# Kernel optimization log

Measured on AMD Instinct MI355X. Metric: run time of the kernel, lower is better.

## Reference

```python
import jax, jax.numpy as jnp
import numpy as np

B, T, C, H = 2, 2048, 768, 12
D = C // H              # head_dim = 64
LOCAL_WINDOW = 256
LN_EPS = 1e-5


def _layernorm(x, w, b):
    mu = jnp.mean(x, axis=-1, keepdims=True)
    var = jnp.var(x, axis=-1, keepdims=True)
    return (x - mu) * jax.lax.rsqrt(var + LN_EPS) * w + b


def setup_inputs() -> dict:
    key = jax.random.key(0)
    ks = jax.random.split(key, 8)
    inp = {
        "x": jax.random.normal(ks[0], (B, T, C), dtype=jnp.float32),
        "mamba_raw": jax.random.normal(ks[1], (B, T, C), dtype=jnp.float32),
        # c_attn / c_proj per nn.init in __init__
        "c_attn_w": 0.02 * jax.random.normal(ks[2], (C, 3 * C), dtype=jnp.float32),
        "c_attn_b": jnp.zeros((3 * C,), dtype=jnp.float32),
        "c_proj_w": 0.02 * jax.random.normal(ks[3], (C, C), dtype=jnp.float32),
        "c_proj_b": jnp.zeros((C,), dtype=jnp.float32),
        "ln_w": jnp.ones((C,), dtype=jnp.float32),
        "ln_b": jnp.zeros((C,), dtype=jnp.float32),
        "mamba_scale": jnp.asarray(0.1, dtype=jnp.float32),
        "sel_w": 0.01 * jax.random.normal(ks[4], (C, 1), dtype=jnp.float32),
        "sel_b": jnp.zeros((1,), dtype=jnp.float32),
        "local_weight": jnp.asarray(0.5, dtype=jnp.float32),
        "global_weight": jnp.asarray(0.5, dtype=jnp.float32),
    }
    return inp


def reference(x, mamba_raw, c_attn_w, c_attn_b, c_proj_w, c_proj_b,
              ln_w, ln_b, mamba_scale, sel_w, sel_b, local_weight, global_weight):
    scale = D ** -0.5
    qkv = x @ c_attn_w + c_attn_b                       # (B,T,3C)
    q, k, v = jnp.split(qkv, 3, axis=-1)
    q = q.reshape(B, T, H, D)
    k = k.reshape(B, T, H, D)
    v = v.reshape(B, T, H, D)

    scores = jnp.einsum('bihd,bjhd->bhij', q, k) * scale  # (B,H,T,T)
    i = jnp.arange(T)[:, None]
    j = jnp.arange(T)[None, :]
    causal = j > i                                       # mask strictly-future keys
    neg_inf = jnp.asarray(-jnp.inf, dtype=scores.dtype)
    scores = jnp.where(causal, neg_inf, scores)

    # frozen mamba branch (mamba_raw is a constant activation)
    mamba_raw = jax.lax.stop_gradient(mamba_raw)
    mamba_scaled = mamba_scale * _layernorm(mamba_raw, ln_w, ln_b)   # (B,T,C)
    sel = jax.nn.sigmoid(mamba_scaled @ sel_w + sel_b)               # (B,T,1)
    sel = sel[:, None, :, 0][:, :, None, :]                          # (B,1,1,T) over keys

    attn_global = scores * (0.5 + 0.5 * sel)             # -inf stays -inf

    outside_local = j < jnp.maximum(i - LOCAL_WINDOW, 0)
    attn_local = jnp.where(outside_local, neg_inf, scores)

    w_l = jax.nn.sigmoid(local_weight)
    w_g = jax.nn.sigmoid(global_weight)
    w_sum = w_l + w_g
    w_l, w_g = w_l / w_sum, w_g / w_sum

    attn_combined = w_l * jax.nn.softmax(attn_local, axis=-1) \
                  + w_g * jax.nn.softmax(attn_global, axis=-1)

    out = jnp.einsum('bhij,bjhd->bihd', attn_combined, v).reshape(B, T, C)
    return out @ c_proj_w + c_proj_b
```

## Files before the change

### kernel.cpp

```cpp
#include <hip/hip_runtime.h>
#include <math.h>

#define Bsz 2
#define Tsz 2048
#define Csz 768
#define Hsz 12
#define C3  2304
#define WIN 256
#define LN_EPS 1e-5f

#define QSCALE 0.1803368801111137f

typedef short bf16x8 __attribute__((ext_vector_type(8)));
typedef float f32x4  __attribute__((ext_vector_type(4)));

__device__ __forceinline__ unsigned short f2b(float f) {
    unsigned int u = __float_as_uint(f);
    u = (u + 0x7fffu + ((u >> 16) & 1u)) >> 16;
    return (unsigned short)u;
}

__device__ __forceinline__ float fast_exp2(float x) {
    float r;
    asm("v_exp_f32 %0, %1" : "=v"(r) : "v"(x));
    return r;
}

__global__ __launch_bounds__(256) void prep_fused(
    const float* __restrict__ x, unsigned short* __restrict__ xb,
    const float* __restrict__ c_attn_w, unsigned short* __restrict__ wq,
    const float* __restrict__ c_proj_w, unsigned short* __restrict__ wp,
    const float* __restrict__ mr, const float* __restrict__ ln_w,
    const float* __restrict__ ln_b, const float* __restrict__ scale_p,
    const float* __restrict__ sel_w, const float* __restrict__ sel_b,
    float* __restrict__ sel)
{
    __shared__ float tile[32][33];
    __shared__ float red1[256];
    __shared__ float red2[256];
    __shared__ float mu_sh, rstd_sh;

    const int blk = blockIdx.x;
    const int tid = threadIdx.x;

    if (blk < 3072) {
        int idx = blk * 256 + tid;
        float4 v = *(const float4*)(x + (size_t)idx * 4);
        unsigned int lo = (unsigned int)f2b(v.x) | ((unsigned int)f2b(v.y) << 16);
        unsigned int hi = (unsigned int)f2b(v.z) | ((unsigned int)f2b(v.w) << 16);
        uint2 o; o.x = lo; o.y = hi;
        *(uint2*)(xb + (size_t)idx * 4) = o;
        return;
    }
    if (blk < 5376) {
        const float* src; unsigned short* dst; int K, N, n0, k0;
        if (blk < 4800) {
            int i = blk - 3072;
            src = c_attn_w; dst = wq; K = Csz; N = C3;
            n0 = (i % 72) * 32; k0 = (i / 72) * 32;
        } else {
            int i = blk - 4800;
            src = c_proj_w; dst = wp; K = Csz; N = Csz;
            n0 = (i % 24) * 32; k0 = (i / 24) * 32;
        }
        const int tx = tid & 31, ty = tid >> 5;
        #pragma unroll
        for (int p = 0; p < 4; ++p)
            tile[ty + p * 8][tx] = src[(size_t)(k0 + ty + p * 8) * N + n0 + tx];
        __syncthreads();
        #pragma unroll
        for (int p = 0; p < 4; ++p)
            dst[(size_t)(n0 + ty + p * 8) * K + k0 + tx] = f2b(tile[tx][ty + p * 8]);
        return;
    }

    const int r = blk - 5376;
    const float* row = mr + (size_t)r * Csz;

    float s = 0.f, s2 = 0.f;
    for (int c = tid; c < Csz; c += 256) {
        float xv = row[c];
        s += xv; s2 += xv * xv;
    }
    red1[tid] = s; red2[tid] = s2;
    __syncthreads();
    for (int st = 128; st > 0; st >>= 1) {
        if (tid < st) { red1[tid] += red1[tid + st]; red2[tid] += red2[tid + st]; }
        __syncthreads();
    }
    if (tid == 0) {
        float mu = red1[0] * (1.f / Csz);
        float var = red2[0] * (1.f / Csz) - mu * mu;
        mu_sh = mu;
        rstd_sh = rsqrtf(var + LN_EPS);
    }
    __syncthreads();
    const float mu = mu_sh, rstd = rstd_sh;

    float dot = 0.f;
    for (int c = tid; c < Csz; c += 256) {
        float xn = (row[c] - mu) * rstd * ln_w[c] + ln_b[c];
        dot += xn * sel_w[c];
    }
    red1[tid] = dot;
    __syncthreads();
    for (int st = 128; st > 0; st >>= 1) {
        if (tid < st) red1[tid] += red1[tid + st];
        __syncthreads();
    }
    if (tid == 0) {
        float z = scale_p[0] * red1[0] + sel_b[0];
        sel[r] = 0.5f + 0.5f / (1.f + __expf(-z));
    }
}

template<int MODE>
__global__ __launch_bounds__(256) void gemm_bt_mfma(
    const unsigned short* __restrict__ A, const unsigned short* __restrict__ BT,
    const float* __restrict__ bias, void* __restrict__ Cout,
    unsigned short* __restrict__ KP, unsigned short* __restrict__ VP,
    int M, int N, int K)
{
    __shared__ unsigned short As[128 * 32];
    __shared__ unsigned short Bs[128 * 32];

    const int tid = threadIdx.x;
    const int lane = tid & 63, widx = tid >> 6;
    const int lm = lane & 15, quad = lane >> 4;
    const int wm = widx >> 1, wn = widx & 1;
    const int m0 = blockIdx.y * 128, n0 = blockIdx.x * 128;

    f32x4 acc[4][4];
    #pragma unroll
    for (int mt = 0; mt < 4; ++mt)
        #pragma unroll
        for (int nt = 0; nt < 4; ++nt)
            acc[mt][nt] = f32x4{0.f, 0.f, 0.f, 0.f};

    int rowS[2], cS[2];
    #pragma unroll
    for (int t = 0; t < 2; ++t) {
        int idx = t * 256 + tid;
        rowS[t] = idx >> 2;
        cS[t] = idx & 3;
    }

    bf16x8 pa[2], pb[2];
    #pragma unroll
    for (int t = 0; t < 2; ++t) {
        pa[t] = *(const bf16x8*)(A + (size_t)(m0 + rowS[t]) * K + cS[t] * 8);
        pb[t] = *(const bf16x8*)(BT + (size_t)(n0 + rowS[t]) * K + cS[t] * 8);
    }

    const int nk = K / 32;
    for (int kt = 0; kt < nk; ++kt) {
        __syncthreads();
        #pragma unroll
        for (int t = 0; t < 2; ++t) {
            *(bf16x8*)(&As[rowS[t] * 32 + ((cS[t] ^ ((rowS[t] >> 1) & 3)) << 3)]) = pa[t];
            *(bf16x8*)(&Bs[rowS[t] * 32 + ((cS[t] ^ ((rowS[t] >> 1) & 3)) << 3)]) = pb[t];
        }
        __syncthreads();
        if (kt + 1 < nk) {
            int k0 = (kt + 1) * 32;
            #pragma unroll
            for (int t = 0; t < 2; ++t) {
                pa[t] = *(const bf16x8*)(A + (size_t)(m0 + rowS[t]) * K + k0 + cS[t] * 8);
                pb[t] = *(const bf16x8*)(BT + (size_t)(n0 + rowS[t]) * K + k0 + cS[t] * 8);
            }
        }
        bf16x8 af[4], bf[4];
        #pragma unroll
        for (int mt = 0; mt < 4; ++mt) {
            int m = wm * 64 + mt * 16 + lm;
            af[mt] = *(const bf16x8*)(&As[m * 32 + ((quad ^ ((m >> 1) & 3)) << 3)]);
        }
        #pragma unroll
        for (int nt = 0; nt < 4; ++nt) {
            int n = wn * 64 + nt * 16 + lm;
            bf[nt] = *(const bf16x8*)(&Bs[n * 32 + ((quad ^ ((n >> 1) & 3)) << 3)]);
        }
        #pragma unroll
        for (int mt = 0; mt < 4; ++mt)
            #pragma unroll
            for (int nt = 0; nt < 4; ++nt)
                acc[mt][nt] = __builtin_amdgcn_mfma_f32_16x16x32_bf16(
                    af[mt], bf[nt], acc[mt][nt], 0, 0, 0);
    }

    float bv[4];
    #pragma unroll
    for (int nt = 0; nt < 4; ++nt)
        bv[nt] = bias[n0 + wn * 64 + nt * 16 + lm];

    #pragma unroll
    for (int mt = 0; mt < 4; ++mt) {
        #pragma unroll
        for (int nt = 0; nt < 4; ++nt) {
            const int cb = n0 + wn * 64 + nt * 16;
            const int col = cb + lm;
            const int rbase = m0 + wm * 64 + mt * 16 + quad * 4;
            if (MODE == 0) {
                #pragma unroll
                for (int r = 0; r < 4; ++r)
                    ((float*)Cout)[(size_t)(rbase + r) * N + col] =
                        acc[mt][nt][r] + bv[nt];
            } else if (cb < Csz) {
                #pragma unroll
                for (int r = 0; r < 4; ++r)
                    ((unsigned short*)Cout)[(size_t)(rbase + r) * Csz + col] =
                        f2b((acc[mt][nt][r] + bv[nt]) * QSCALE);
            } else if (cb < 2 * Csz) {
                const int dfull = col - Csz;
                const int h = dfull >> 6, dd = dfull & 63;
                const int f = dd >> 5, qd = (dd >> 3) & 3, j = dd & 7;
                #pragma unroll
                for (int r = 0; r < 4; ++r) {
                    const int row = rbase + r;
                    const int b = row >> 11, t = row & 2047;
                    const int ktk = t >> 4, lmk = t & 15;
                    size_t addr = ((((size_t)((b * Hsz + h) * 128 + ktk)) * 2 + f) * 512)
                                  + (qd * 16 + lmk) * 8 + j;
                    KP[addr] = f2b(acc[mt][nt][r] + bv[nt]);
                }
            } else {
                const int dfull = col - 2 * Csz;
                const int h = dfull >> 6, dd = dfull & 63;
                const int ntv = dd >> 4, lmv = dd & 15;
                #pragma unroll
                for (int r = 0; r < 4; ++r) {
                    const int row = rbase + r;
                    const int b = row >> 11, t = row & 2047;
                    const int jtv = t >> 5, qv = (t >> 3) & 3, j = t & 7;
                    size_t addr = (((size_t)((b * Hsz + h) * 64 + jtv) * 4 + ntv) * 512)
                                  + (qv * 16 + lmv) * 8 + j;
                    VP[addr] = f2b(acc[mt][nt][r] + bv[nt]);
                }
            }
        }
    }
}

__global__ __launch_bounds__(256) void attn_mfma(
    const unsigned short* __restrict__ qb, const unsigned short* __restrict__ KP,
    const unsigned short* __restrict__ VP, const float* __restrict__ fsel_arr,
    const float* __restrict__ lw_p, const float* __restrict__ gw_p,
    unsigned short* __restrict__ attnb)
{
    __shared__ __align__(16) unsigned char SMEM[18432];

    const int tid = threadIdx.x;
    const int widx = tid >> 6, lane = tid & 63;
    const int lm = lane & 15, quad = lane >> 4;

    unsigned short* Pg = (unsigned short*)SMEM + (widx * 2 + 0) * (16 * 72);
    unsigned short* Pl = (unsigned short*)SMEM + (widx * 2 + 1) * (16 * 72);
    float* MrgF = (float*)SMEM;
    #define MRG(slot, br, row, col) MrgF[((((slot) * 2 + (br)) * 16 + (row)) * 66) + (col)]

    const int strip = 127 - (int)(blockIdx.x / 24);
    const int bh = (int)(blockIdx.x % 24);
    const int h = bh % Hsz, b = bh / Hsz;
    const int i0 = strip * 16;

    const unsigned short* KPb = KP + (size_t)bh * 131072 + lane * 8;
    const unsigned short* VPb = VP + (size_t)bh * 131072 + lane * 8;

    const unsigned short* qrow =
        qb + (size_t)(b * Tsz + i0 + lm) * Csz + h * 64 + quad * 8;
    const bf16x8 qf0 = *(const bf16x8*)qrow;
    const bf16x8 qf1 = *(const bf16x8*)(qrow + 32);

    float l_g[4], l_l[4];
    f32x4 Og[4], Ol[4];
    #pragma unroll
    for (int r = 0; r < 4; ++r) { l_g[r] = 0.f; l_l[r] = 0.f; }
    #pragma unroll
    for (int nt = 0; nt < 4; ++nt) {
        Og[nt] = f32x4{0.f, 0.f, 0.f, 0.f};
        Ol[nt] = f32x4{0.f, 0.f, 0.f, 0.f};
    }

    const int jtd = i0 >> 6;
    const int jtl = (jtd - 4) > 0 ? (jtd - 4) : 0;

    for (int jt = widx; jt <= jtd; jt += 4) {
        const int j0 = jt * 64;
        const bool diag = (jt == jtd);
        const bool firstloc = (jt == jtl) && !diag;
        const bool loc = (jt >= jtl);

        const unsigned short* kp = KPb + (size_t)(j0 >> 4) * 1024;
        bf16x8 kc0[4], kc1[4];
        #pragma unroll
        for (int nt = 0; nt < 4; ++nt) {
            kc0[nt] = *(const bf16x8*)(kp + nt * 1024);
            kc1[nt] = *(const bf16x8*)(kp + nt * 1024 + 512);
        }

        f32x4 s[4];
        #pragma unroll
        for (int nt = 0; nt < 4; ++nt) {
            f32x4 z = f32x4{0.f, 0.f, 0.f, 0.f};
            z = __builtin_amdgcn_mfma_f32_16x16x32_bf16(qf0, kc0[nt], z, 0, 0, 0);
            z = __builtin_amdgcn_mfma_f32_16x16x32_bf16(qf1, kc1[nt], z, 0, 0, 0);
            s[nt] = z;
        }

        float fs[4];
        #pragma unroll
        for (int nt = 0; nt < 4; ++nt)
            fs[nt] = fsel_arr[b * Tsz + j0 + nt * 16 + lm];

        if (diag) {
            #pragma unroll
            for (int r = 0; r < 4; ++r) {
                const int qi = i0 + quad * 4 + r;
                #pragma unroll
                for (int nt = 0; nt < 4; ++nt) {
                    const int kj = j0 + nt * 16 + lm;
                    float p = fast_exp2(s[nt][r] * fs[nt]);
                    p = (kj > qi) ? 0.f : p;
                    unsigned int u = __float_as_uint(p);
                    l_g[r] += __uint_as_float(u & 0xffff0000u);
                    Pg[(quad * 4 + r) * 72 + nt * 16 + lm] = (unsigned short)(u >> 16);
                }
            }
        } else {
            #pragma unroll
            for (int r = 0; r < 4; ++r)
                #pragma unroll
                for (int nt = 0; nt < 4; ++nt) {
                    float p = fast_exp2(s[nt][r] * fs[nt]);
                    unsigned int u = __float_as_uint(p);
                    l_g[r] += __uint_as_float(u & 0xffff0000u);
                    Pg[(quad * 4 + r) * 72 + nt * 16 + lm] = (unsigned short)(u >> 16);
                }
        }

        if (loc) {
            if (diag) {
                #pragma unroll
                for (int r = 0; r < 4; ++r) {
                    const int qi = i0 + quad * 4 + r;
                    #pragma unroll
                    for (int nt = 0; nt < 4; ++nt) {
                        const int kj = j0 + nt * 16 + lm;
                        float p = fast_exp2(s[nt][r]);
                        p = (kj > qi || kj < qi - WIN) ? 0.f : p;
                        unsigned int u = __float_as_uint(p);
                        l_l[r] += __uint_as_float(u & 0xffff0000u);
                        Pl[(quad * 4 + r) * 72 + nt * 16 + lm] = (unsigned short)(u >> 16);
                    }
                }
            } else if (firstloc) {
                #pragma unroll
                for (int r = 0; r < 4; ++r) {
                    const int qi = i0 + quad * 4 + r;
                    #pragma unroll
                    for (int nt = 0; nt < 4; ++nt) {
                        const int kj = j0 + nt * 16 + lm;
                        float p = fast_exp2(s[nt][r]);
                        p = (kj < qi - WIN) ? 0.f : p;
                        unsigned int u = __float_as_uint(p);
                        l_l[r] += __uint_as_float(u & 0xffff0000u);
                        Pl[(quad * 4 + r) * 72 + nt * 16 + lm] = (unsigned short)(u >> 16);
                    }
                }
            } else {
                #pragma unroll
                for (int r = 0; r < 4; ++r)
                    #pragma unroll
                    for (int nt = 0; nt < 4; ++nt) {
                        float p = fast_exp2(s[nt][r]);
                        unsigned int u = __float_as_uint(p);
                        l_l[r] += __uint_as_float(u & 0xffff0000u);
                        Pl[(quad * 4 + r) * 72 + nt * 16 + lm] = (unsigned short)(u >> 16);
                    }
            }
        }

        const bf16x8 ag0 = *(const bf16x8*)(&Pg[lm * 72 + quad * 8]);
        const bf16x8 ag1 = *(const bf16x8*)(&Pg[lm * 72 + 32 + quad * 8]);
        bf16x8 al0 = {}, al1 = {};
        if (loc) {
            al0 = *(const bf16x8*)(&Pl[lm * 72 + quad * 8]);
            al1 = *(const bf16x8*)(&Pl[lm * 72 + 32 + quad * 8]);
        }

        const unsigned short* vp = VPb + (size_t)(j0 >> 5) * 2048;
        #pragma unroll
        for (int nt = 0; nt < 4; ++nt) {
            bf16x8 v0 = *(const bf16x8*)(vp + nt * 512);
            bf16x8 v1 = *(const bf16x8*)(vp + 2048 + nt * 512);
            Og[nt] = __builtin_amdgcn_mfma_f32_16x16x32_bf16(ag0, v0, Og[nt], 0, 0, 0);
            Og[nt] = __builtin_amdgcn_mfma_f32_16x16x32_bf16(ag1, v1, Og[nt], 0, 0, 0);
            if (loc) {
                Ol[nt] = __builtin_amdgcn_mfma_f32_16x16x32_bf16(al0, v0, Ol[nt], 0, 0, 0);
                Ol[nt] = __builtin_amdgcn_mfma_f32_16x16x32_bf16(al1, v1, Ol[nt], 0, 0, 0);
            }
        }
    }

    #pragma unroll
    for (int st = 1; st < 16; st <<= 1) {
        #pragma unroll
        for (int r = 0; r < 4; ++r) {
            l_g[r] += __shfl_xor(l_g[r], st);
            l_l[r] += __shfl_xor(l_l[r], st);
        }
    }

    auto write_slot = [&](int slot) {
        #pragma unroll
        for (int r = 0; r < 4; ++r) {
            const int row = quad * 4 + r;
            #pragma unroll
            for (int nt = 0; nt < 4; ++nt) {
                MRG(slot, 0, row, nt * 16 + lm) = Og[nt][r];
                MRG(slot, 1, row, nt * 16 + lm) = Ol[nt][r];
            }
            if (lm == 0) {
                MRG(slot, 0, row, 65) = l_g[r];
                MRG(slot, 1, row, 65) = l_l[r];
            }
        }
    };
    auto combine_slot = [&](int slot) {
        #pragma unroll
        for (int r = 0; r < 4; ++r) {
            const int row = quad * 4 + r;
            {
                l_g[r] += MRG(slot, 0, row, 65);
                #pragma unroll
                for (int nt = 0; nt < 4; ++nt)
                    Og[nt][r] += MRG(slot, 0, row, nt * 16 + lm);
            }
            {
                l_l[r] += MRG(slot, 1, row, 65);
                #pragma unroll
                for (int nt = 0; nt < 4; ++nt)
                    Ol[nt][r] += MRG(slot, 1, row, nt * 16 + lm);
            }
        }
    };

    __syncthreads();
    if (widx == 1) write_slot(0);
    if (widx == 3) write_slot(1);
    __syncthreads();
    if (widx == 0) combine_slot(0);
    if (widx == 2) combine_slot(1);
    __syncthreads();
    if (widx == 2) write_slot(0);
    __syncthreads();

    if (widx == 0) {
        combine_slot(0);

        float wl = 1.f / (1.f + __expf(-lw_p[0]));
        float wg = 1.f / (1.f + __expf(-gw_p[0]));
        float ws = wl + wg;
        wl /= ws; wg /= ws;

        #pragma unroll
        for (int r = 0; r < 4; ++r) {
            const int row = quad * 4 + r;
            const float cg = wg / l_g[r];
            const float cl = wl / l_l[r];
            #pragma unroll
            for (int nt = 0; nt < 4; ++nt) {
                float v = Og[nt][r] * cg + Ol[nt][r] * cl;
                attnb[(size_t)(b * Tsz + i0 + row) * Csz + h * 64 + nt * 16 + lm] =
                    f2b(v);
            }
        }
    }
    #undef MRG
}

extern "C" void kernel_launch(void* const* d_in, const int* in_sizes, int n_in,
                              void* d_out, int out_size, void* d_ws, size_t ws_size,
                              hipStream_t stream)
{
    const float* x          = (const float*)d_in[0];
    const float* mamba_raw  = (const float*)d_in[1];
    const float* c_attn_w   = (const float*)d_in[2];
    const float* c_attn_b   = (const float*)d_in[3];
    const float* c_proj_w   = (const float*)d_in[4];
    const float* c_proj_b   = (const float*)d_in[5];
    const float* ln_w       = (const float*)d_in[6];
    const float* ln_b       = (const float*)d_in[7];
    const float* mamba_sc   = (const float*)d_in[8];
    const float* sel_w      = (const float*)d_in[9];
    const float* sel_b      = (const float*)d_in[10];
    const float* local_w    = (const float*)d_in[11];
    const float* global_w   = (const float*)d_in[12];
    float* out = (float*)d_out;

    const int M = Bsz * Tsz;

    unsigned short* xb    = (unsigned short*)d_ws;
    unsigned short* wq    = xb + (size_t)M * Csz;
    unsigned short* wp    = wq + (size_t)C3 * Csz;
    unsigned short* qb    = wp + (size_t)Csz * Csz;
    unsigned short* kpb   = qb + (size_t)M * Csz;
    unsigned short* vpb   = kpb + (size_t)24 * 131072;
    unsigned short* attnb = vpb + (size_t)24 * 131072;
    float* sel = (float*)(attnb + (size_t)M * Csz);

    prep_fused<<<9472, 256, 0, stream>>>(x, xb, c_attn_w, wq, c_proj_w, wp,
                                         mamba_raw, ln_w, ln_b, mamba_sc,
                                         sel_w, sel_b, sel);

    {
        dim3 g(C3 / 128, M / 128);
        gemm_bt_mfma<1><<<g, 256, 0, stream>>>(xb, wq, c_attn_b, qb,
                                               kpb, vpb, M, C3, Csz);
    }

    attn_mfma<<<128 * Hsz * Bsz, 256, 0, stream>>>(qb, kpb, vpb, sel,
                                                   local_w, global_w, attnb);

    {
        dim3 g(Csz / 128, M / 128);
        gemm_bt_mfma<0><<<g, 256, 0, stream>>>(attnb, wp, c_proj_b, out,
                                               nullptr, nullptr, M, Csz, Csz);
    }
}
```

Baseline: 192.8 us.

## Write K/V row-major from QKV GEMM, pack in separate kernel, fold LN/selector into GEMM

The QKV GEMM epilogue no longer does scattered 2-byte stores into the MFMA-packed K/V layouts. It writes K and V contiguously into a row-major buffer, and a new pack kernel rearranges them with vectorized 16-byte copies (V transposed through LDS). The layernorm/selector rows and the c_proj weight transpose move from the prep kernel into extra blocks of the QKV GEMM launch, so they run alongside it. This adds a kernel launch and an extra round trip of K/V through memory in exchange for coalesced GEMM stores and a lighter prep kernel.

```diff
diff --git a/kernel.cpp b/kernel.cpp
--- a/kernel.cpp
+++ b/kernel.cpp
@@ -28,17 +28,9 @@
 
 __global__ __launch_bounds__(256) void prep_fused(
     const float* __restrict__ x, unsigned short* __restrict__ xb,
-    const float* __restrict__ c_attn_w, unsigned short* __restrict__ wq,
-    const float* __restrict__ c_proj_w, unsigned short* __restrict__ wp,
-    const float* __restrict__ mr, const float* __restrict__ ln_w,
-    const float* __restrict__ ln_b, const float* __restrict__ scale_p,
-    const float* __restrict__ sel_w, const float* __restrict__ sel_b,
-    float* __restrict__ sel)
+    const float* __restrict__ c_attn_w, unsigned short* __restrict__ wq)
 {
     __shared__ float tile[32][33];
-    __shared__ float red1[256];
-    __shared__ float red2[256];
-    __shared__ float mu_sh, rstd_sh;
 
     const int blk = blockIdx.x;
     const int tid = threadIdx.x;
@@ -52,83 +44,148 @@
         *(uint2*)(xb + (size_t)idx * 4) = o;
         return;
     }
-    if (blk < 5376) {
-        const float* src; unsigned short* dst; int K, N, n0, k0;
-        if (blk < 4800) {
-            int i = blk - 3072;
-            src = c_attn_w; dst = wq; K = Csz; N = C3;
-            n0 = (i % 72) * 32; k0 = (i / 72) * 32;
-        } else {
-            int i = blk - 4800;
-            src = c_proj_w; dst = wp; K = Csz; N = Csz;
-            n0 = (i % 24) * 32; k0 = (i / 24) * 32;
-        }
-        const int tx = tid & 31, ty = tid >> 5;
-        #pragma unroll
-        for (int p = 0; p < 4; ++p)
-            tile[ty + p * 8][tx] = src[(size_t)(k0 + ty + p * 8) * N + n0 + tx];
-        __syncthreads();
-        #pragma unroll
-        for (int p = 0; p < 4; ++p)
-            dst[(size_t)(n0 + ty + p * 8) * K + k0 + tx] = f2b(tile[tx][ty + p * 8]);
+    int i = blk - 3072;
+    const int n0 = (i % 72) * 32, k0 = (i / 72) * 32;
+    const int tx = tid & 31, ty = tid >> 5;
+    #pragma unroll
+    for (int p = 0; p < 4; ++p)
+        tile[ty + p * 8][tx] = c_attn_w[(size_t)(k0 + ty + p * 8) * C3 + n0 + tx];
+    __syncthreads();
+    #pragma unroll
+    for (int p = 0; p < 4; ++p)
+        wq[(size_t)(n0 + ty + p * 8) * Csz + k0 + tx] = f2b(tile[tx][ty + p * 8]);
+}
+
+__global__ __launch_bounds__(256) void pack_fused(
+    const unsigned short* __restrict__ kvb, unsigned short* __restrict__ KP,
+    unsigned short* __restrict__ VP)
+{
+    __shared__ unsigned short tile[32][72];
+
+    if (blockIdx.x < 1536) {
+        const int g = blockIdx.x * 4 + (threadIdx.x >> 6);
+        const int lane = threadIdx.x & 63;
+        const int lm = lane & 15, quad = lane >> 4;
+        const int f = g & 1;
+        const int kt = (g >> 1) & 127;
+        const int bh = g >> 8;
+        const int b = bh / Hsz, h = bh % Hsz;
+        const unsigned short* src = kvb +
+            (size_t)(b * Tsz + kt * 16 + lm) * 1536 + h * 64 + f * 32 + quad * 8;
+        bf16x8 v = *(const bf16x8*)src;
+        *(bf16x8*)(KP + (size_t)g * 512 + lane * 8) = v;
         return;
     }
 
-    const int r = blk - 5376;
-    const float* row = mr + (size_t)r * Csz;
-
-    float s = 0.f, s2 = 0.f;
-    for (int c = tid; c < Csz; c += 256) {
-        float xv = row[c];
-        s += xv; s2 += xv * xv;
-    }
-    red1[tid] = s; red2[tid] = s2;
+    const int g = blockIdx.x - 1536;
+    const int jt = g & 63;
+    const int bh = g >> 6;
+    const int b = bh / Hsz, h = bh % Hsz;
+
+    const int row = threadIdx.x >> 3, dc = (threadIdx.x & 7) * 8;
+    *(bf16x8*)&tile[row][dc] = *(const bf16x8*)(
+        kvb + (size_t)(b * Tsz + jt * 32 + row) * 1536 + Csz + h * 64 + dc);
     __syncthreads();
-    for (int st = 128; st > 0; st >>= 1) {
-        if (tid < st) { red1[tid] += red1[tid + st]; red2[tid] += red2[tid + st]; }
-        __syncthreads();
-    }
-    if (tid == 0) {
-        float mu = red1[0] * (1.f / Csz);
-        float var = red2[0] * (1.f / Csz) - mu * mu;
-        mu_sh = mu;
-        rstd_sh = rsqrtf(var + LN_EPS);
-    }
-    __syncthreads();
-    const float mu = mu_sh, rstd = rstd_sh;
-
-    float dot = 0.f;
-    for (int c = tid; c < Csz; c += 256) {
-        float xn = (row[c] - mu) * rstd * ln_w[c] + ln_b[c];
-        dot += xn * sel_w[c];
-    }
-    red1[tid] = dot;
-    __syncthreads();
-    for (int st = 128; st > 0; st >>= 1) {
-        if (tid < st) red1[tid] += red1[tid + st];
-        __syncthreads();
-    }
-    if (tid == 0) {
-        float z = scale_p[0] * red1[0] + sel_b[0];
-        sel[r] = 0.5f + 0.5f / (1.f + __expf(-z));
-    }
+
+    const int lane = threadIdx.x & 63, nt = threadIdx.x >> 6;
+    const int lm = lane & 15, quad = lane >> 4;
+    unsigned short tmp[8];
+    #pragma unroll
+    for (int j = 0; j < 8; ++j) tmp[j] = tile[quad * 8 + j][nt * 16 + lm];
+    *(bf16x8*)(VP + ((size_t)(bh * 64 + jt) * 4 + nt) * 512 + lane * 8) =
+        *(bf16x8*)tmp;
 }
 
 template<int MODE>
 __global__ __launch_bounds__(256) void gemm_bt_mfma(
     const unsigned short* __restrict__ A, const unsigned short* __restrict__ BT,
     const float* __restrict__ bias, void* __restrict__ Cout,
-    unsigned short* __restrict__ KP, unsigned short* __restrict__ VP,
+    unsigned short* __restrict__ kvb,
+    const float* __restrict__ mr, const float* __restrict__ ln_w,
+    const float* __restrict__ ln_b, const float* __restrict__ scale_p,
+    const float* __restrict__ sel_w, const float* __restrict__ sel_b,
+    float* __restrict__ sel,
+    const float* __restrict__ c_proj_w, unsigned short* __restrict__ wp,
     int M, int N, int K)
 {
-    __shared__ unsigned short As[128 * 32];
-    __shared__ unsigned short Bs[128 * 32];
+    __shared__ __align__(16) unsigned char SM[2 * 128 * 32 * 2];
+    unsigned short* As = (unsigned short*)SM;
+    unsigned short* Bs = As + 128 * 32;
 
     const int tid = threadIdx.x;
+    int bx, by;
+    if (MODE == 1) {
+        const int bid = blockIdx.x;
+        if (bid >= 4672) {
+            float (*tile)[33] = (float(*)[33])SM;
+            int i = bid - 4672;
+            const int n0 = (i % 24) * 32, k0 = (i / 24) * 32;
+            const int tx = tid & 31, ty = tid >> 5;
+            #pragma unroll
+            for (int p = 0; p < 4; ++p)
+                tile[ty + p * 8][tx] =
+                    c_proj_w[(size_t)(k0 + ty + p * 8) * Csz + n0 + tx];
+            __syncthreads();
+            #pragma unroll
+            for (int p = 0; p < 4; ++p)
+                wp[(size_t)(n0 + ty + p * 8) * Csz + k0 + tx] =
+                    f2b(tile[tx][ty + p * 8]);
+            return;
+        }
+        if (bid >= 576) {
+            float* red1 = (float*)SM;
+            float* red2 = red1 + 256;
+            float* mu_p = red2 + 256;
+            const int r = bid - 576;
+            const float* row = mr + (size_t)r * Csz;
+
+            float s = 0.f, s2 = 0.f;
+            for (int c = tid; c < Csz; c += 256) {
+                float xv = row[c];
+                s += xv; s2 += xv * xv;
+            }
+            red1[tid] = s; red2[tid] = s2;
+            __syncthreads();
+            for (int st = 128; st > 0; st >>= 1) {
+                if (tid < st) { red1[tid] += red1[tid + st]; red2[tid] += red2[tid + st]; }
+                __syncthreads();
+            }
+            if (tid == 0) {
+                float mu = red1[0] * (1.f / Csz);
+                float var = red2[0] * (1.f / Csz) - mu * mu;
+                mu_p[0] = mu;
+                mu_p[1] = rsqrtf(var + LN_EPS);
+            }
+            __syncthreads();
+            const float mu = mu_p[0], rstd = mu_p[1];
+
+            float dot = 0.f;
+            for (int c = tid; c < Csz; c += 256) {
+                float xn = (row[c] - mu) * rstd * ln_w[c] + ln_b[c];
+                dot += xn * sel_w[c];
+            }
+            __syncthreads();
+            red1[tid] = dot;
+            __syncthreads();
+            for (int st = 128; st > 0; st >>= 1) {
+                if (tid < st) red1[tid] += red1[tid + st];
+                __syncthreads();
+            }
+            if (tid == 0) {
+                float z = scale_p[0] * red1[0] + sel_b[0];
+                sel[r] = 0.5f + 0.5f / (1.f + __expf(-z));
+            }
+            return;
+        }
+        bx = bid % 18; by = bid / 18;
+    } else {
+        bx = blockIdx.x; by = blockIdx.y;
+    }
+
     const int lane = tid & 63, widx = tid >> 6;
     const int lm = lane & 15, quad = lane >> 4;
     const int wm = widx >> 1, wn = widx & 1;
-    const int m0 = blockIdx.y * 128, n0 = blockIdx.x * 128;
+    const int m0 = by * 128, n0 = bx * 128;
 
     f32x4 acc[4][4];
     #pragma unroll
@@ -210,32 +267,11 @@
                 for (int r = 0; r < 4; ++r)
                     ((unsigned short*)Cout)[(size_t)(rbase + r) * Csz + col] =
                         f2b((acc[mt][nt][r] + bv[nt]) * QSCALE);
-            } else if (cb < 2 * Csz) {
-                const int dfull = col - Csz;
-                const int h = dfull >> 6, dd = dfull & 63;
-                const int f = dd >> 5, qd = (dd >> 3) & 3, j = dd & 7;
-                #pragma unroll
-                for (int r = 0; r < 4; ++r) {
-                    const int row = rbase + r;
-                    const int b = row >> 11, t = row & 2047;
-                    const int ktk = t >> 4, lmk = t & 15;
-                    size_t addr = ((((size_t)((b * Hsz + h) * 128 + ktk)) * 2 + f) * 512)
-                                  + (qd * 16 + lmk) * 8 + j;
-                    KP[addr] = f2b(acc[mt][nt][r] + bv[nt]);
-                }
             } else {
-                const int dfull = col - 2 * Csz;
-                const int h = dfull >> 6, dd = dfull & 63;
-                const int ntv = dd >> 4, lmv = dd & 15;
-                #pragma unroll
-                for (int r = 0; r < 4; ++r) {
-                    const int row = rbase + r;
-                    const int b = row >> 11, t = row & 2047;
-                    const int jtv = t >> 5, qv = (t >> 3) & 3, j = t & 7;
-                    size_t addr = (((size_t)((b * Hsz + h) * 64 + jtv) * 4 + ntv) * 512)
-                                  + (qv * 16 + lmv) * 8 + j;
-                    VP[addr] = f2b(acc[mt][nt][r] + bv[nt]);
-                }
+                #pragma unroll
+                for (int r = 0; r < 4; ++r)
+                    kvb[(size_t)(rbase + r) * 1536 + col - Csz] =
+                        f2b(acc[mt][nt][r] + bv[nt]);
             }
         }
     }
@@ -504,20 +540,20 @@
     unsigned short* wq    = xb + (size_t)M * Csz;
     unsigned short* wp    = wq + (size_t)C3 * Csz;
     unsigned short* qb    = wp + (size_t)Csz * Csz;
-    unsigned short* kpb   = qb + (size_t)M * Csz;
+    unsigned short* kvb   = qb + (size_t)M * Csz;
+    unsigned short* kpb   = kvb + (size_t)M * 1536;
     unsigned short* vpb   = kpb + (size_t)24 * 131072;
     unsigned short* attnb = vpb + (size_t)24 * 131072;
     float* sel = (float*)(attnb + (size_t)M * Csz);
 
-    prep_fused<<<9472, 256, 0, stream>>>(x, xb, c_attn_w, wq, c_proj_w, wp,
-                                         mamba_raw, ln_w, ln_b, mamba_sc,
-                                         sel_w, sel_b, sel);
-
-    {
-        dim3 g(C3 / 128, M / 128);
-        gemm_bt_mfma<1><<<g, 256, 0, stream>>>(xb, wq, c_attn_b, qb,
-                                               kpb, vpb, M, C3, Csz);
-    }
+    prep_fused<<<4800, 256, 0, stream>>>(x, xb, c_attn_w, wq);
+
+    gemm_bt_mfma<1><<<5248, 256, 0, stream>>>(
+        xb, wq, c_attn_b, qb, kvb,
+        mamba_raw, ln_w, ln_b, mamba_sc, sel_w, sel_b, sel,
+        c_proj_w, wp, M, C3, Csz);
+
+    pack_fused<<<3072, 256, 0, stream>>>(kvb, kpb, vpb);
 
     attn_mfma<<<128 * Hsz * Bsz, 256, 0, stream>>>(qb, kpb, vpb, sel,
                                                    local_w, global_w, attnb);
@@ -525,6 +561,9 @@
     {
         dim3 g(Csz / 128, M / 128);
         gemm_bt_mfma<0><<<g, 256, 0, stream>>>(attnb, wp, c_proj_b, out,
+                                               nullptr,
+                                               nullptr, nullptr, nullptr, nullptr,
+                                               nullptr, nullptr, nullptr,
                                                nullptr, nullptr, M, Csz, Csz);
     }
 }
```

Result: slower. 201.4 us (+4.5%).
